# Performance work log

Hardware: AMD Instinct MI355X
Metric: run time of the kernel (lower is better)

The kernel has to match this reference:

```python
import jax, jax.numpy as jnp
import numpy as np

E = 512
H = 8
D = E // H
WIN = 128  # mask_window_size


def setup_inputs() -> dict:
    key = jax.random.key(0)
    k1, k2, k3, k4, k5 = jax.random.split(key, 5)
    B, L = 2, 4096
    s = 1.0 / np.sqrt(E)
    return {
        "x": jax.random.normal(k1, (B, L, E), dtype=jnp.float32),
        "in_proj_w": jax.random.normal(k2, (3 * E, E), dtype=jnp.float32) * s,
        "in_proj_b": jax.random.normal(k3, (3 * E,), dtype=jnp.float32) * 0.02,
        "out_w": jax.random.normal(k4, (E, E), dtype=jnp.float32) * s,
        "out_b": jax.random.normal(k5, (E,), dtype=jnp.float32) * 0.02,
    }


def reference(x, in_proj_w, in_proj_b, out_w, out_b):
    B, L, _ = x.shape
    # fused qkv projection (torch MultiheadAttention in_proj): x @ W.T + b
    qkv = jnp.einsum("ble,fe->blf", x, in_proj_w) + in_proj_b  # [B,L,3E]
    q, k, v = jnp.split(qkv, 3, axis=-1)
    # [B,H,L,D]
    q = q.reshape(B, L, H, D).transpose(0, 2, 1, 3)
    k = k.reshape(B, L, H, D).transpose(0, 2, 1, 3)
    v = v.reshape(B, L, H, D).transpose(0, 2, 1, 3)
    scores = jnp.einsum("bhqd,bhkd->bhqk", q, k) / jnp.sqrt(jnp.float32(D))
    # (diagonal stays blocked — faithful to the original gen_mask quirk)
    idx = jnp.arange(L)
    dist = jnp.abs(idx[:, None] - idx[None, :])
    blocked = (dist > WIN) | (dist == 0)  # [L,L]
    scores = jnp.where(blocked[None, None], -jnp.inf, scores)
    attn = jax.nn.softmax(scores, axis=-1)  # [B,H,L,L]
    out = jnp.einsum("bhqk,bhkd->bhqd", attn, v)  # [B,H,L,D]
    out = out.transpose(0, 2, 1, 3).reshape(B, L, E)
    return jnp.einsum("ble,fe->blf", out, out_w) + out_b
```

## Files before the change

kernel.cpp:

```cpp
#include <hip/hip_runtime.h>
#include <math.h>

#define E_DIM 512
#define H_DIM 8
#define WIN 128
#define L_SEQ 4096
#define B_SZ 2

typedef unsigned short ushort_t;
typedef unsigned int uint_t;
typedef __attribute__((ext_vector_type(8))) __bf16 bf16x8;
typedef __attribute__((ext_vector_type(4))) float f32x4;

__device__ __forceinline__ ushort_t f2bf(float f) {
    uint_t u = __float_as_uint(f);
    u = u + 0x7fffu + ((u >> 16) & 1u);
    return (ushort_t)(u >> 16);
}
__device__ __forceinline__ float bf2f(ushort_t h) {
    return __uint_as_float((uint_t)h << 16);
}

__device__ __forceinline__ void gload16(const ushort_t* g, ushort_t* l) {
    __builtin_amdgcn_global_load_lds(
        (const __attribute__((address_space(1))) void*)g,
        (__attribute__((address_space(3))) void*)l,
        16, 0, 0);
}


__global__ __launch_bounds__(256) void convertX(
    const float* __restrict__ x,  ushort_t* __restrict__ xh,
    const float* __restrict__ w1, ushort_t* __restrict__ w1h,
    const float* __restrict__ w2, ushort_t* __restrict__ w2h) {
    int sg = blockIdx.x * 256 + threadIdx.x;
    const float* src; ushort_t* dh;
    if (sg < 524288)      { src = x;  dh = xh; }
    else if (sg < 622592) { src = w1; dh = w1h; sg -= 524288; }
    else                  { src = w2; dh = w2h; sg -= 622592; }
    const int tile = sg >> 6, slot = sg & 63;
    const int row = (tile >> 4) * 16 + (slot & 15);
    const int k   = (tile & 15) * 32 + (slot >> 4) * 8;
    const float4 v0 = *(const float4*)&src[(size_t)row * 512 + k];
    const float4 v1 = *(const float4*)&src[(size_t)row * 512 + k + 4];
    const float vv[8] = {v0.x, v0.y, v0.z, v0.w, v1.x, v1.y, v1.z, v1.w};
    union { ushort_t u[8]; ushort4 v[2]; } h;
    #pragma unroll
    for (int j = 0; j < 8; j++) h.u[j] = f2bf(vv[j]);
    ((ushort4*)(dh + (size_t)sg * 8))[0] = h.v[0];
    ((ushort4*)(dh + (size_t)sg * 8))[1] = h.v[1];
}

__global__ __launch_bounds__(256) void gemm_qkv(
    const ushort_t* __restrict__ Ah,
    const ushort_t* __restrict__ Wh,
    const float* __restrict__ bias,
    ushort_t* __restrict__ qTh,
    ushort_t* __restrict__ kTh,
    ushort_t* __restrict__ vTh) {
    __shared__ __align__(16) ushort_t sAh[2][8 * 512];
    __shared__ __align__(16) ushort_t sWh[2][8 * 512];

    const int tid = threadIdx.x, lane = tid & 63, w = tid >> 6;
    const int wm = w & 1, wn = w >> 1, ln = lane & 15, quad = lane >> 4;
    const int bx = blockIdx.x, by = blockIdx.y;
    const int lo8 = lane * 8;
    const int wu = __builtin_amdgcn_readfirstlane(w);

    f32x4 acc[4][4];
    const f32x4 zero = {0.f, 0.f, 0.f, 0.f};
    #pragma unroll
    for (int i = 0; i < 4; i++)
        #pragma unroll
        for (int j = 0; j < 4; j++) acc[i][j] = zero;

    const ushort_t* pb[4];
    ushort_t* db0[4];
    ushort_t* db1[4];
    #pragma unroll
    for (int t = 0; t < 4; t++) {
        const int g = wu * 4 + t;
        if (g < 8) {
            pb[t] = Ah + ((size_t)(bx * 8 + g) * 16) * 512;
            db0[t] = &sAh[0][g * 512]; db1[t] = &sAh[1][g * 512];
        } else {
            const int u = g - 8;
            pb[t] = Wh + ((size_t)(by * 8 + u) * 16) * 512;
            db0[t] = &sWh[0][u * 512]; db1[t] = &sWh[1][u * 512];
        }
    }

    #pragma unroll
    for (int t = 0; t < 4; t++)
        gload16(pb[t] + lo8, db0[t]);

    for (int kt = 0; kt < 16; kt++) {
        __syncthreads();
        if (kt < 15) {
            const int koff = (kt + 1) * 512;
            if ((kt + 1) & 1) {
                #pragma unroll
                for (int t = 0; t < 4; t++) gload16(pb[t] + koff + lo8, db1[t]);
            } else {
                #pragma unroll
                for (int t = 0; t < 4; t++) gload16(pb[t] + koff + lo8, db0[t]);
            }
        }
        const int cb = kt & 1;
        bf16x8 fah[4];
        #pragma unroll
        for (int i = 0; i < 4; i++)
            fah[i] = *(const bf16x8*)&sAh[cb][(wm * 4 + i) * 512 + lo8];
        #pragma unroll
        for (int j = 0; j < 4; j++) {
            const bf16x8 fbh = *(const bf16x8*)&sWh[cb][(wn * 4 + j) * 512 + lo8];
            #pragma unroll
            for (int i = 0; i < 4; i++)
                acc[i][j] = __builtin_amdgcn_mfma_f32_16x16x32_bf16(fah[i], fbh, acc[i][j], 0, 0, 0);
        }
    }

    const int b = bx >> 5;
    const int h = 2 * (by & 3) + wn;
    if (by < 8) {
        ushort_t* dh = (by < 4) ? qTh : kTh;
        #pragma unroll
        for (int i = 0; i < 4; i++) {
            const int rt = (bx & 31) * 8 + wm * 4 + i;
            const size_t tb = ((size_t)(b * 8 + h) * 256 + rt) * 2;
            #pragma unroll
            for (int j = 0; j < 4; j++) {
                const float bv = bias[by * 128 + wn * 64 + j * 16 + ln];
                const size_t tile = tb + (j >> 1);
                #pragma unroll
                for (int r = 0; r < 4; r++) {
                    const int slot = ((j * 2 + (ln >> 3)) & 3) * 16 + quad * 4 + r;
                    const size_t idx = tile * 512 + slot * 8 + (ln & 7);
                    dh[idx] = f2bf(acc[i][j][r] + bv);
                }
            }
        }
    } else {
        const int kwin = (bx & 31) * 2 + wm;
        #pragma unroll
        for (int i = 0; i < 4; i++) {
            const int kk = i >> 1;
            #pragma unroll
            for (int j = 0; j < 4; j++) {
                const float bv = bias[by * 128 + wn * 64 + j * 16 + ln];
                const size_t tile = (((size_t)(b * 8 + h) * 64 + kwin) * 4 + j) * 2 + kk;
                #pragma unroll
                for (int r = 0; r < 4; r++) {
                    const int klq = quad * 4 + r;
                    const int slot = ((i & 1) * 2 + (klq >> 3)) * 16 + ln;
                    const size_t idx = tile * 512 + slot * 8 + (klq & 7);
                    vTh[idx] = f2bf(acc[i][j][r] + bv);
                }
            }
        }
    }
}

__global__ __launch_bounds__(512) void attn_mfma(
    const ushort_t* __restrict__ qTh,
    const ushort_t* __restrict__ kTh,
    const ushort_t* __restrict__ vTh,
    ushort_t* __restrict__ outh) {
    __shared__ __align__(16) ushort_t sKh[2][8 * 512];
    __shared__ __align__(16) ushort_t sV [2][8 * 512];
    __shared__ __align__(16) ushort_t sP [16 * 512];

    const int qs = blockIdx.x * 128;
    const int h = blockIdx.y, b = blockIdx.z;
    const int bh = b * 8 + h;
    const int tid = threadIdx.x, lane = tid & 63;
    const int w = tid >> 6, ln = lane & 15, quad = lane >> 4;
    const int lo8 = lane * 8;

    bf16x8 qf[2];
    {
        const size_t qt = ((size_t)bh * 256 + (qs >> 4) + w) * 2;
        qf[0] = *(const bf16x8*)(qTh + (qt + 0) * 512 + lo8);
        qf[1] = *(const bf16x8*)(qTh + (qt + 1) * 512 + lo8);
    }

    f32x4 oacc[4];
    const f32x4 zero = {0.f, 0.f, 0.f, 0.f};
    #pragma unroll
    for (int dt = 0; dt < 4; dt++) oacc[dt] = zero;
    float m_run = -1e30f, l_run = 0.f;

    const float cscale = 0.125f * 1.44269504f;
    const int qlo = qs + 16 * w;
    const int q = qlo + ln;

    {
        if (w < 4) {
            int st = (qs >> 4) - 8 + w;
            st = st < 0 ? 0 : (st > 255 ? 255 : st);
            const size_t kb = ((size_t)bh * 256 + st) * 2 * 512 + lo8;
            gload16(kTh + kb,       &sKh[0][(w * 2 + 0) * 512]);
            gload16(kTh + kb + 512, &sKh[0][(w * 2 + 1) * 512]);
        } else {
            const int u = w - 4;
            int vw = (qs >> 6) - 2;
            vw = vw < 0 ? 0 : (vw > 63 ? 63 : vw);
            const size_t vb = (((size_t)bh * 64 + vw) * 4 + u) * 2 * 512 + lo8;
            gload16(vTh + vb,       &sV[0][(u * 2 + 0) * 512]);
            gload16(vTh + vb + 512, &sV[0][(u * 2 + 1) * 512]);
        }
    }

    for (int kt = 0; kt < 6; kt++) {
        const int ks = qs - 128 + kt * 64;

        __syncthreads();

        if (kt < 5) {
            const int nb = (kt + 1) & 1;
            if (w < 4) {
                int st = (qs >> 4) - 8 + (kt + 1) * 4 + w;
                st = st < 0 ? 0 : (st > 255 ? 255 : st);
                const size_t kb = ((size_t)bh * 256 + st) * 2 * 512 + lo8;
                gload16(kTh + kb,       &sKh[nb][(w * 2 + 0) * 512]);
                gload16(kTh + kb + 512, &sKh[nb][(w * 2 + 1) * 512]);
            } else {
                const int u = w - 4;
                int vw = (qs >> 6) - 2 + kt + 1;
                vw = vw < 0 ? 0 : (vw > 63 ? 63 : vw);
                const size_t vb = (((size_t)bh * 64 + vw) * 4 + u) * 2 * 512 + lo8;
                gload16(vTh + vb,       &sV[nb][(u * 2 + 0) * 512]);
                gload16(vTh + vb + 512, &sV[nb][(u * 2 + 1) * 512]);
            }
        }
        const int cb = kt & 1;

        bool dead[4];
        #pragma unroll
        for (int jt = 0; jt < 4; jt++) {
            const int klo = ks + 16 * jt;
            dead[jt] = (klo > qlo + 15 + WIN) || (klo + 15 < qlo - WIN) ||
                       (klo >= L_SEQ) || (klo + 15 < 0);
        }
        const bool ktAlive = !(dead[0] && dead[1] && dead[2] && dead[3]);

        if (ktAlive) {
            f32x4 st4[4];
            #pragma unroll
            for (int jt = 0; jt < 4; jt++) {
                f32x4 a = zero;
                if (!dead[jt]) {
                    #pragma unroll
                    for (int kk = 0; kk < 2; kk++) {
                        const bf16x8 kh = *(const bf16x8*)&sKh[cb][(jt * 2 + kk) * 512 + lo8];
                        a = __builtin_amdgcn_mfma_f32_16x16x32_bf16(kh, qf[kk], a, 0, 0, 0);
                    }
                }
                st4[jt] = a;
            }

            float uv[4][4];
            float mk = -INFINITY;
            #pragma unroll
            for (int jt = 0; jt < 4; jt++) {
                if (!dead[jt]) {
                    #pragma unroll
                    for (int r = 0; r < 4; r++) {
                        const int kcol = ks + jt * 16 + quad * 4 + r;
                        const int dist = q > kcol ? q - kcol : kcol - q;
                        const bool ok = (kcol >= 0) && (kcol < L_SEQ) && (dist >= 1) && (dist <= WIN);
                        const float val = ok ? st4[jt][r] * cscale : -INFINITY;
                        uv[jt][r] = val;
                        mk = fmaxf(mk, val);
                    }
                }
            }
            mk = fmaxf(mk, __shfl_xor(mk, 16));
            mk = fmaxf(mk, __shfl_xor(mk, 32));

            const float mnew = fmaxf(m_run, mk);
            const float alpha = exp2f(m_run - mnew);
            m_run = mnew;

            float ps = 0.f;
            #pragma unroll
            for (int jt = 0; jt < 4; jt++) {
                if (!dead[jt]) {
                    #pragma unroll
                    for (int r = 0; r < 4; r++) {
                        const float pv = exp2f(uv[jt][r] - mnew);
                        uv[jt][r] = pv;
                        ps += pv;
                    }
                }
            }
            ps += __shfl_xor(ps, 16);
            ps += __shfl_xor(ps, 32);
            l_run = l_run * alpha + ps;

            float ar[4];
            #pragma unroll
            for (int r = 0; r < 4; r++)
                ar[r] = __shfl(alpha, quad * 4 + r);
            #pragma unroll
            for (int dt = 0; dt < 4; dt++)
                #pragma unroll
                for (int r = 0; r < 4; r++)
                    oacc[dt][r] *= ar[r];

            #pragma unroll
            for (int jt = 0; jt < 4; jt++) {
                ushort4 pw;
                if (!dead[jt]) {
                    pw.x = f2bf(uv[jt][0]); pw.y = f2bf(uv[jt][1]);
                    pw.z = f2bf(uv[jt][2]); pw.w = f2bf(uv[jt][3]);
                } else {
                    pw.x = 0; pw.y = 0; pw.z = 0; pw.w = 0;
                }
                const int slot = ((jt & 1) * 2 + (quad >> 1)) * 16 + ln;
                *(ushort4*)&sP[w * 1024 + (jt >> 1) * 512 + slot * 8 + (quad & 1) * 4] = pw;
            }

            #pragma unroll
            for (int kk = 0; kk < 2; kk++) {
                const bf16x8 pf = *(const bf16x8*)&sP[w * 1024 + kk * 512 + lo8];
                #pragma unroll
                for (int dt = 0; dt < 4; dt++) {
                    const bf16x8 vf = *(const bf16x8*)&sV[cb][(dt * 2 + kk) * 512 + lo8];
                    oacc[dt] = __builtin_amdgcn_mfma_f32_16x16x32_bf16(pf, vf, oacc[dt], 0, 0, 0);
                }
            }
        }
    }

    const int Rt = ((b * L_SEQ + qs) >> 4) + w;
    #pragma unroll
    for (int r = 0; r < 4; r++) {
        const float lr = __shfl(l_run, quad * 4 + r);
        const float inv_l = 1.f / lr;
        #pragma unroll
        for (int dt = 0; dt < 4; dt++) {
            const float v = oacc[dt][r] * inv_l;
            const int tile = Rt * 16 + h * 2 + (dt >> 1);
            const int slot = ((dt & 1) * 2 + (ln >> 3)) * 16 + quad * 4 + r;
            const size_t idx = (size_t)tile * 512 + slot * 8 + (ln & 7);
            outh[idx] = f2bf(v);
        }
    }
}

__global__ __launch_bounds__(512) void gemm_out(
    const ushort_t* __restrict__ Ah,
    const ushort_t* __restrict__ Wh,
    const float* __restrict__ bias, float* __restrict__ C) {
    __shared__ __align__(16) ushort_t sAh[2][16 * 512];
    __shared__ __align__(16) ushort_t sWh[2][8 * 512];

    const int tid = threadIdx.x, lane = tid & 63, w = tid >> 6;
    const int wm = w & 3, wn = w >> 2, ln = lane & 15, quad = lane >> 4;
    const int bx = blockIdx.x, by = blockIdx.y;
    const int lo8 = lane * 8;
    const int wu = __builtin_amdgcn_readfirstlane(w);

    f32x4 acc[2][2];
    const f32x4 zero = {0.f, 0.f, 0.f, 0.f};
    #pragma unroll
    for (int i = 0; i < 2; i++)
        #pragma unroll
        for (int j = 0; j < 2; j++) acc[i][j] = zero;

    const ushort_t* pb[3];
    ushort_t* db0[3];
    ushort_t* db1[3];
    #pragma unroll
    for (int t = 0; t < 3; t++) {
        const int g = wu * 3 + t;
        if (g < 16) {
            pb[t] = Ah + ((size_t)(bx * 8 + (g >> 1)) * 16 + (g & 1)) * 512;
            db0[t] = &sAh[0][g * 512]; db1[t] = &sAh[1][g * 512];
        } else {
            const int u = g - 16;
            pb[t] = Wh + ((size_t)(by * 4 + (u >> 1)) * 16 + (u & 1)) * 512;
            db0[t] = &sWh[0][u * 512]; db1[t] = &sWh[1][u * 512];
        }
    }

    #pragma unroll
    for (int t = 0; t < 3; t++)
        gload16(pb[t] + lo8, db0[t]);

    for (int KT = 0; KT < 8; KT++) {
        __syncthreads();
        if (KT < 7) {
            const int koff = (KT + 1) * 1024;
            if ((KT + 1) & 1) {
                #pragma unroll
                for (int t = 0; t < 3; t++) gload16(pb[t] + koff + lo8, db1[t]);
            } else {
                #pragma unroll
                for (int t = 0; t < 3; t++) gload16(pb[t] + koff + lo8, db0[t]);
            }
        }
        const int cb = KT & 1;
        #pragma unroll
        for (int ks = 0; ks < 2; ks++) {
            bf16x8 fah[2];
            #pragma unroll
            for (int i = 0; i < 2; i++)
                fah[i] = *(const bf16x8*)&sAh[cb][((wm * 2 + i) * 2 + ks) * 512 + lo8];
            #pragma unroll
            for (int j = 0; j < 2; j++) {
                const bf16x8 fbh = *(const bf16x8*)&sWh[cb][((wn * 2 + j) * 2 + ks) * 512 + lo8];
                #pragma unroll
                for (int i = 0; i < 2; i++)
                    acc[i][j] = __builtin_amdgcn_mfma_f32_16x16x32_bf16(fah[i], fbh, acc[i][j], 0, 0, 0);
            }
        }
    }

    #pragma unroll
    for (int i = 0; i < 2; i++) {
        const int row0 = bx * 128 + wm * 32 + i * 16 + quad * 4;
        #pragma unroll
        for (int j = 0; j < 2; j++) {
            const int col = by * 64 + wn * 32 + j * 16 + ln;
            const float bv = bias[col];
            #pragma unroll
            for (int r = 0; r < 4; r++)
                C[(size_t)(row0 + r) * E_DIM + col] = acc[i][j][r] + bv;
        }
    }
}

extern "C" void kernel_launch(void* const* d_in, const int* in_sizes, int n_in,
                              void* d_out, int out_size, void* d_ws, size_t ws_size,
                              hipStream_t stream) {
    const float* x         = (const float*)d_in[0];
    const float* in_proj_w = (const float*)d_in[1];
    const float* in_proj_b = (const float*)d_in[2];
    const float* out_w     = (const float*)d_in[3];
    const float* out_b     = (const float*)d_in[4];
    float* out = (float*)d_out;

    const int N = B_SZ * L_SEQ;
    const size_t NE = (size_t)N * E_DIM;

    char* p = (char*)d_ws;
    ushort_t* xh  = (ushort_t*)p; p += NE * 2;
    ushort_t* w1h = (ushort_t*)p; p += (size_t)3 * E_DIM * E_DIM * 2;
    ushort_t* w2h = (ushort_t*)p; p += (size_t)E_DIM * E_DIM * 2;
    ushort_t* qTh = (ushort_t*)p; p += NE * 2;
    ushort_t* kTh = (ushort_t*)p; p += NE * 2;
    ushort_t* vTh = (ushort_t*)p; p += NE * 2;
    ushort_t* ath = (ushort_t*)p; p += NE * 2;

    convertX<<<2560, 256, 0, stream>>>(x, xh, in_proj_w, w1h, out_w, w2h);

    gemm_qkv<<<dim3(64, 12), 256, 0, stream>>>(
        xh, w1h, in_proj_b, qTh, kTh, vTh);

    attn_mfma<<<dim3(L_SEQ / 128, H_DIM, B_SZ), 512, 0, stream>>>(
        qTh, kTh, vTh, ath);

    gemm_out<<<dim3(64, 8), 512, 0, stream>>>(
        ath, w2h, out_b, out);
}
```

Before: 130.4 us.

## Use packed bf16 conversion, skip dead half-tiles and conditional rescale in attention

New measurement: 130.6 us. No clear change (+0.1%).

```diff
diff --git a/kernel.cpp b/kernel.cpp
--- a/kernel.cpp
+++ b/kernel.cpp
@@ -17,8 +17,10 @@
     u = u + 0x7fffu + ((u >> 16) & 1u);
     return (ushort_t)(u >> 16);
 }
-__device__ __forceinline__ float bf2f(ushort_t h) {
-    return __uint_as_float((uint_t)h << 16);
+__device__ __forceinline__ uint_t pk2bf(float lo, float hi) {
+    uint_t r;
+    asm("v_cvt_pk_bf16_f32 %0, %1, %2" : "=v"(r) : "v"(lo), "v"(hi));
+    return r;
 }
 
 __device__ __forceinline__ void gload16(const ushort_t* g, ushort_t* l) {
@@ -43,12 +45,12 @@
     const int k   = (tile & 15) * 32 + (slot >> 4) * 8;
     const float4 v0 = *(const float4*)&src[(size_t)row * 512 + k];
     const float4 v1 = *(const float4*)&src[(size_t)row * 512 + k + 4];
-    const float vv[8] = {v0.x, v0.y, v0.z, v0.w, v1.x, v1.y, v1.z, v1.w};
-    union { ushort_t u[8]; ushort4 v[2]; } h;
-    #pragma unroll
-    for (int j = 0; j < 8; j++) h.u[j] = f2bf(vv[j]);
-    ((ushort4*)(dh + (size_t)sg * 8))[0] = h.v[0];
-    ((ushort4*)(dh + (size_t)sg * 8))[1] = h.v[1];
+    uint4 ov;
+    ov.x = pk2bf(v0.x, v0.y);
+    ov.y = pk2bf(v0.z, v0.w);
+    ov.z = pk2bf(v1.x, v1.y);
+    ov.w = pk2bf(v1.z, v1.w);
+    *(uint4*)(dh + (size_t)sg * 8) = ov;
 }
 
 __global__ __launch_bounds__(256) void gemm_qkv(
@@ -132,12 +134,14 @@
             for (int j = 0; j < 4; j++) {
                 const float bv = bias[by * 128 + wn * 64 + j * 16 + ln];
                 const size_t tile = tb + (j >> 1);
-                #pragma unroll
-                for (int r = 0; r < 4; r++) {
-                    const int slot = ((j * 2 + (ln >> 3)) & 3) * 16 + quad * 4 + r;
-                    const size_t idx = tile * 512 + slot * 8 + (ln & 7);
-                    dh[idx] = f2bf(acc[i][j][r] + bv);
-                }
+                const uint_t pa = pk2bf(acc[i][j][0] + bv, acc[i][j][1] + bv);
+                const uint_t pc = pk2bf(acc[i][j][2] + bv, acc[i][j][3] + bv);
+                const int slot0 = ((j * 2 + (ln >> 3)) & 3) * 16 + quad * 4;
+                const size_t idx0 = tile * 512 + slot0 * 8 + (ln & 7);
+                dh[idx0]      = (ushort_t)pa;
+                dh[idx0 + 8]  = (ushort_t)(pa >> 16);
+                dh[idx0 + 16] = (ushort_t)pc;
+                dh[idx0 + 24] = (ushort_t)(pc >> 16);
             }
         }
     } else {
@@ -149,13 +153,11 @@
             for (int j = 0; j < 4; j++) {
                 const float bv = bias[by * 128 + wn * 64 + j * 16 + ln];
                 const size_t tile = (((size_t)(b * 8 + h) * 64 + kwin) * 4 + j) * 2 + kk;
-                #pragma unroll
-                for (int r = 0; r < 4; r++) {
-                    const int klq = quad * 4 + r;
-                    const int slot = ((i & 1) * 2 + (klq >> 3)) * 16 + ln;
-                    const size_t idx = tile * 512 + slot * 8 + (klq & 7);
-                    vTh[idx] = f2bf(acc[i][j][r] + bv);
-                }
+                const uint_t pa = pk2bf(acc[i][j][0] + bv, acc[i][j][1] + bv);
+                const uint_t pc = pk2bf(acc[i][j][2] + bv, acc[i][j][3] + bv);
+                const int slot = ((i & 1) * 2 + (quad >> 1)) * 16 + ln;
+                uint2 ov; ov.x = pa; ov.y = pc;
+                *(uint2*)&vTh[tile * 512 + slot * 8 + (quad & 1) * 4] = ov;
             }
         }
     }
@@ -193,6 +195,8 @@
     const float cscale = 0.125f * 1.44269504f;
     const int qlo = qs + 16 * w;
     const int q = qlo + ln;
+    const int lo_b = (q - WIN) < 0 ? 0 : (q - WIN);
+    const int hi_b = (q + WIN) > (L_SEQ - 1) ? (L_SEQ - 1) : (q + WIN);
 
     {
         if (w < 4) {
@@ -242,10 +246,13 @@
             dead[jt] = (klo > qlo + 15 + WIN) || (klo + 15 < qlo - WIN) ||
                        (klo >= L_SEQ) || (klo + 15 < 0);
         }
-        const bool ktAlive = !(dead[0] && dead[1] && dead[2] && dead[3]);
+        const bool hdead0 = dead[0] && dead[1];
+        const bool hdead1 = dead[2] && dead[3];
+        const bool ktAlive = !(hdead0 && hdead1);
 
         if (ktAlive) {
             f32x4 st4[4];
+            __builtin_amdgcn_s_setprio(1);
             #pragma unroll
             for (int jt = 0; jt < 4; jt++) {
                 f32x4 a = zero;
@@ -258,39 +265,35 @@
                 }
                 st4[jt] = a;
             }
-
-            float uv[4][4];
-            float mk = -INFINITY;
+            __builtin_amdgcn_s_setprio(0);
+
+            float mkr = -INFINITY;
+            #pragma unroll
+            for (int jt = 0; jt < 4; jt++)
+                if (!dead[jt])
+                    #pragma unroll
+                    for (int r = 0; r < 4; r++)
+                        mkr = fmaxf(mkr, st4[jt][r]);
+            mkr = fmaxf(mkr, __shfl_xor(mkr, 16));
+            mkr = fmaxf(mkr, __shfl_xor(mkr, 32));
+
+            const float mnew = fmaxf(m_run, mkr * cscale);
+            const bool raised = mnew > m_run;
+            const float alpha = exp2f(m_run - mnew);
+            m_run = mnew;
+
+            float ps = 0.f;
             #pragma unroll
             for (int jt = 0; jt < 4; jt++) {
                 if (!dead[jt]) {
                     #pragma unroll
                     for (int r = 0; r < 4; r++) {
                         const int kcol = ks + jt * 16 + quad * 4 + r;
-                        const int dist = q > kcol ? q - kcol : kcol - q;
-                        const bool ok = (kcol >= 0) && (kcol < L_SEQ) && (dist >= 1) && (dist <= WIN);
-                        const float val = ok ? st4[jt][r] * cscale : -INFINITY;
-                        uv[jt][r] = val;
-                        mk = fmaxf(mk, val);
-                    }
-                }
-            }
-            mk = fmaxf(mk, __shfl_xor(mk, 16));
-            mk = fmaxf(mk, __shfl_xor(mk, 32));
-
-            const float mnew = fmaxf(m_run, mk);
-            const float alpha = exp2f(m_run - mnew);
-            m_run = mnew;
-
-            float ps = 0.f;
-            #pragma unroll
-            for (int jt = 0; jt < 4; jt++) {
-                if (!dead[jt]) {
-                    #pragma unroll
-                    for (int r = 0; r < 4; r++) {
-                        const float pv = exp2f(uv[jt][r] - mnew);
-                        uv[jt][r] = pv;
-                        ps += pv;
+                        const bool ok = (kcol >= lo_b) && (kcol <= hi_b) && (kcol != q);
+                        float p = exp2f(st4[jt][r] * cscale - mnew);
+                        p = ok ? p : 0.f;
+                        st4[jt][r] = p;
+                        ps += p;
                     }
                 }
             }
@@ -298,54 +301,67 @@
             ps += __shfl_xor(ps, 32);
             l_run = l_run * alpha + ps;
 
-            float ar[4];
-            #pragma unroll
-            for (int r = 0; r < 4; r++)
-                ar[r] = __shfl(alpha, quad * 4 + r);
-            #pragma unroll
-            for (int dt = 0; dt < 4; dt++)
+            if (__any(raised)) {
+                float ar[4];
                 #pragma unroll
                 for (int r = 0; r < 4; r++)
-                    oacc[dt][r] *= ar[r];
+                    ar[r] = __shfl(alpha, quad * 4 + r);
+                #pragma unroll
+                for (int dt = 0; dt < 4; dt++)
+                    #pragma unroll
+                    for (int r = 0; r < 4; r++)
+                        oacc[dt][r] *= ar[r];
+            }
 
             #pragma unroll
             for (int jt = 0; jt < 4; jt++) {
-                ushort4 pw;
-                if (!dead[jt]) {
-                    pw.x = f2bf(uv[jt][0]); pw.y = f2bf(uv[jt][1]);
-                    pw.z = f2bf(uv[jt][2]); pw.w = f2bf(uv[jt][3]);
-                } else {
-                    pw.x = 0; pw.y = 0; pw.z = 0; pw.w = 0;
+                const bool hd = (jt < 2) ? hdead0 : hdead1;
+                if (!hd) {
+                    uint2 pw;
+                    if (!dead[jt]) {
+                        pw.x = pk2bf(st4[jt][0], st4[jt][1]);
+                        pw.y = pk2bf(st4[jt][2], st4[jt][3]);
+                    } else { pw.x = 0u; pw.y = 0u; }
+                    const int slot = ((jt & 1) * 2 + (quad >> 1)) * 16 + ln;
+                    *(uint2*)&sP[w * 1024 + (jt >> 1) * 512 + slot * 8 + (quad & 1) * 4] = pw;
                 }
-                const int slot = ((jt & 1) * 2 + (quad >> 1)) * 16 + ln;
-                *(ushort4*)&sP[w * 1024 + (jt >> 1) * 512 + slot * 8 + (quad & 1) * 4] = pw;
             }
 
             #pragma unroll
             for (int kk = 0; kk < 2; kk++) {
-                const bf16x8 pf = *(const bf16x8*)&sP[w * 1024 + kk * 512 + lo8];
-                #pragma unroll
-                for (int dt = 0; dt < 4; dt++) {
-                    const bf16x8 vf = *(const bf16x8*)&sV[cb][(dt * 2 + kk) * 512 + lo8];
-                    oacc[dt] = __builtin_amdgcn_mfma_f32_16x16x32_bf16(pf, vf, oacc[dt], 0, 0, 0);
+                const bool hd = (kk == 0) ? hdead0 : hdead1;
+                if (!hd) {
+                    const bf16x8 pf = *(const bf16x8*)&sP[w * 1024 + kk * 512 + lo8];
+                    __builtin_amdgcn_s_setprio(1);
+                    #pragma unroll
+                    for (int dt = 0; dt < 4; dt++) {
+                        const bf16x8 vf = *(const bf16x8*)&sV[cb][(dt * 2 + kk) * 512 + lo8];
+                        oacc[dt] = __builtin_amdgcn_mfma_f32_16x16x32_bf16(pf, vf, oacc[dt], 0, 0, 0);
+                    }
+                    __builtin_amdgcn_s_setprio(0);
                 }
             }
         }
     }
 
     const int Rt = ((b * L_SEQ + qs) >> 4) + w;
+    float invl[4];
     #pragma unroll
     for (int r = 0; r < 4; r++) {
         const float lr = __shfl(l_run, quad * 4 + r);
-        const float inv_l = 1.f / lr;
-        #pragma unroll
-        for (int dt = 0; dt < 4; dt++) {
-            const float v = oacc[dt][r] * inv_l;
-            const int tile = Rt * 16 + h * 2 + (dt >> 1);
-            const int slot = ((dt & 1) * 2 + (ln >> 3)) * 16 + quad * 4 + r;
-            const size_t idx = (size_t)tile * 512 + slot * 8 + (ln & 7);
-            outh[idx] = f2bf(v);
-        }
+        invl[r] = __builtin_amdgcn_rcpf(lr);
+    }
+    #pragma unroll
+    for (int dt = 0; dt < 4; dt++) {
+        const uint_t pa = pk2bf(oacc[dt][0] * invl[0], oacc[dt][1] * invl[1]);
+        const uint_t pc = pk2bf(oacc[dt][2] * invl[2], oacc[dt][3] * invl[3]);
+        const int tile = Rt * 16 + h * 2 + (dt >> 1);
+        const int slot0 = ((dt & 1) * 2 + (ln >> 3)) * 16 + quad * 4;
+        const size_t idx0 = (size_t)tile * 512 + slot0 * 8 + (ln & 7);
+        outh[idx0]      = (ushort_t)pa;
+        outh[idx0 + 8]  = (ushort_t)(pa >> 16);
+        outh[idx0 + 16] = (ushort_t)pc;
+        outh[idx0 + 24] = (ushort_t)(pc >> 16);
     }
 }
 
```
